# Kernel optimization log

Hardware: AMD Instinct MI355X
Metric: run time of the kernel (lower is better)

The kernel has to match this reference:

```python
import jax, jax.numpy as jnp
import numpy as np

D = 128           # volume / particle box size (pixels)
B = 8             # particles per batch
K = 125           # SO(3) grid poses (5x5x5 around each center Euler)
TOPK = 2          # keep_top_k_values
MAX_SHIFT_FRAC = 0.25  # main_config.projmatching.max_shift_fraction


def setup_inputs() -> dict:
    key = jax.random.key(0)
    k1, k2, k3, k4 = jax.random.split(key, 4)
    vol = jax.random.normal(k1, (D, D, D), dtype=jnp.float32)
    parts = jax.random.normal(k2, (B, D, D), dtype=jnp.float32)
    ctf = jax.random.uniform(k3, (B, D, D // 2 + 1), dtype=jnp.float32)
    euler_degs = jax.random.normal(k4, (K, 3), dtype=jnp.float32) * 8.0
    return {"vol": vol, "parts": parts, "ctf": ctf, "euler_degs": euler_degs}


def _rot_z(t):
    c, s = jnp.cos(t), jnp.sin(t)
    z, o = jnp.zeros_like(t), jnp.ones_like(t)
    return jnp.stack([jnp.stack([c, -s, z], -1),
                      jnp.stack([s, c, z], -1),
                      jnp.stack([z, z, o], -1)], -2)


def _rot_y(t):
    c, s = jnp.cos(t), jnp.sin(t)
    z, o = jnp.zeros_like(t), jnp.ones_like(t)
    return jnp.stack([jnp.stack([c, z, s], -1),
                      jnp.stack([z, o, z], -1),
                      jnp.stack([-s, z, c], -1)], -2)


def euler_zyz_to_matrix(degs):
    # RELION Euler convention ZYZ: R = Rz(a) @ Ry(b) @ Rz(c)
    rad = jnp.deg2rad(degs)
    return _rot_z(rad[..., 0]) @ _rot_y(rad[..., 1]) @ _rot_z(rad[..., 2])


def trilinear_sample(vol, zi, yi, xi):
    # vol: (Dz, Dy, W) complex64; coords: (K, h, w) float32 array indices
    Dz, Dy, W = vol.shape
    z0, y0, x0 = jnp.floor(zi), jnp.floor(yi), jnp.floor(xi)
    tz, ty, tx = zi - z0, yi - y0, xi - x0
    out = jnp.zeros(zi.shape, dtype=vol.dtype)
    for dz in (0, 1):
        wz = tz if dz else 1.0 - tz
        zc = z0 + dz
        vz = (zc >= 0) & (zc < Dz)
        zdx = jnp.clip(zc, 0, Dz - 1).astype(jnp.int32)
        for dy in (0, 1):
            wy = ty if dy else 1.0 - ty
            yc = y0 + dy
            vy = (yc >= 0) & (yc < Dy)
            ydx = jnp.clip(yc, 0, Dy - 1).astype(jnp.int32)
            for dx in (0, 1):
                wx = tx if dx else 1.0 - tx
                xc = x0 + dx
                vx = (xc >= 0) & (xc < W)
                xdx = jnp.clip(xc, 0, W - 1).astype(jnp.int32)
                w = jnp.where(vz & vy & vx, wz * wy * wx, 0.0)
                out = out + w * vol[zdx, ydx, xdx]
    return out


def project_fourier(vol_rfft, rotmats):
    # extract_central_slices_rfft: pose-dependent gather+trilinear interp of a
    # central slice from the fftshifted 3D rfft volume. Output: (K, D, D//2+1).
    d = D
    w = d // 2 + 1
    y = jnp.arange(d, dtype=jnp.float32) - d // 2   # fftshifted full-dim freqs (pixel units)
    x = jnp.arange(w, dtype=jnp.float32)            # rfft (non-negative) freqs
    yy, xx = jnp.meshgrid(y, x, indexing='ij')      # (d, w)
    coords = jnp.stack([xx, yy, jnp.zeros_like(yy)], -1)       # xyz, (d, w, 3), z = 0 plane
    rot = jnp.einsum('kij,hwj->khwi', rotmats, coords)          # (K, d, w, 3) rotated xyz
    conj_mask = rot[..., 0] < 0                                  # Hermitian symmetry: flip to x>=0 half
    rot = jnp.where(conj_mask[..., None], -rot, rot)
    xi = rot[..., 0]
    yi = rot[..., 1] + d // 2
    zi = rot[..., 2] + d // 2
    samples = trilinear_sample(vol_rfft, zi, yi, xi)
    samples = jnp.where(conj_mask, jnp.conj(samples), samples)
    r2 = xx ** 2 + yy ** 2                                       # zero beyond Nyquist radius
    samples = jnp.where(r2[None] > (d // 2) ** 2, 0.0, samples)
    return samples


def reference(vol, parts, ctf, euler_degs):
    # compute_dft: rfft volume, fftshift non-rfft dims
    vol_rfft = jnp.fft.fftshift(jnp.fft.rfftn(vol), axes=(0, 1))
    parts_rfft = jnp.fft.fftshift(jnp.fft.rfft2(parts), axes=(-2,))  # (B, D, W)
    rotmats = euler_zyz_to_matrix(euler_degs)                        # (K, 3, 3)
    projs = project_fourier(vol_rfft, rotmats)                       # (K, D, W)
    projs = ctf[:, None] * projs[None]                               # _apply_ctfF: (B, K, D, W)
    # correlate_dft_2d: cross-correlation via iFFT of parts * conj(projs)
    prod = parts_rfft[:, None] * jnp.conj(projs)
    prod = jnp.fft.ifftshift(prod, axes=(-2,))
    corr = jnp.fft.irfft2(prod, s=(D, D))                            # (B, K, D, D)
    corr = jnp.fft.fftshift(corr, axes=(-2, -1))                     # zero shift at center
    # _extract_ccor_max: restrict to |shift| <= max_shift_fraction*D, take top-k peaks
    center = D // 2
    max_shift = int(MAX_SHIFT_FRAC * D)
    idx = jnp.arange(D) - center
    win = (jnp.abs(idx)[:, None] <= max_shift) & (jnp.abs(idx)[None, :] <= max_shift)
    masked = jnp.where(win, corr, -jnp.inf)
    flat = masked.reshape(B, K, D * D)
    vals, top_idx = jax.lax.top_k(flat, TOPK)                        # (B, K, TOPK)
    shifts = jnp.stack([top_idx // D - center, top_idx % D - center], -1)  # (B, K, TOPK, 2) yx
    return vals, shifts
```

## Files before the change

### kernel.cpp

```cpp
#include <hip/hip_runtime.h>
#include <math.h>

#define D 128
#define W 65
#define NK 125
#define NB 8
#define SLAB (D*W)
#define TWO_PI 6.28318530717958647692f
#define R2C 0.70710678118654752440f
#define C8C 0.92387953251128675613f
#define S8C 0.38268343236508977173f
#define ARS 146
#define GRS 131


__device__ __forceinline__ bool better(float va, int ia, float vb, int ib) {
    return (va > vb) || (va == vb && ia < ib);
}
__device__ __forceinline__ float2 cmul(float2 a, float2 b) {
    return make_float2(a.x*b.x - a.y*b.y, a.x*b.y + a.y*b.x);
}
__device__ __forceinline__ void cmac(float2& acc, float2 a, float2 b) {
    acc.x = fmaf(a.x, b.x, fmaf(-a.y, b.y, acc.x));
    acc.y = fmaf(a.x, b.y, fmaf( a.y, b.x, acc.y));
}
__device__ __forceinline__ float2 cadd(float2 a, float2 b){ return make_float2(a.x+b.x, a.y+b.y); }
__device__ __forceinline__ float2 csub(float2 a, float2 b){ return make_float2(a.x-b.x, a.y-b.y); }

__device__ __forceinline__ void fft8_fwd(const float2* x, float2* a) {
    float2 e0 = x[0], o0 = x[1], e1 = x[2], o1 = x[3];
    float2 e2 = x[4], o2 = x[5], e3 = x[6], o3 = x[7];
    float2 t0 = cadd(e0, e2), t1 = csub(e0, e2);
    float2 t2 = cadd(e1, e3), t3 = csub(e1, e3);
    float2 E0 = cadd(t0, t2), E2 = csub(t0, t2);
    float2 E1 = make_float2(t1.x + t3.y, t1.y - t3.x);
    float2 E3 = make_float2(t1.x - t3.y, t1.y + t3.x);
    float2 u0 = cadd(o0, o2), u1 = csub(o0, o2);
    float2 u2 = cadd(o1, o3), u3 = csub(o1, o3);
    float2 O0 = cadd(u0, u2), O2 = csub(u0, u2);
    float2 O1 = make_float2(u1.x + u3.y, u1.y - u3.x);
    float2 O3 = make_float2(u1.x - u3.y, u1.y + u3.x);
    float2 w1 = make_float2(R2C*(O1.x + O1.y), R2C*(O1.y - O1.x));
    float2 w2 = make_float2(O2.y, -O2.x);
    float2 w3 = make_float2(R2C*(O3.y - O3.x), -R2C*(O3.x + O3.y));
    a[0] = cadd(E0, O0); a[4] = csub(E0, O0);
    a[1] = cadd(E1, w1); a[5] = csub(E1, w1);
    a[2] = cadd(E2, w2); a[6] = csub(E2, w2);
    a[3] = cadd(E3, w3); a[7] = csub(E3, w3);
}

__device__ __forceinline__ void ifft8_reg(const float2* x, float2* a) {
    float2 e0 = x[0], o0 = x[1], e1 = x[2], o1 = x[3];
    float2 e2 = x[4], o2 = x[5], e3 = x[6], o3 = x[7];
    float2 t0 = cadd(e0, e2), t1 = csub(e0, e2);
    float2 t2 = cadd(e1, e3), t3 = csub(e1, e3);
    float2 E0 = cadd(t0, t2), E2 = csub(t0, t2);
    float2 E1 = make_float2(t1.x - t3.y, t1.y + t3.x);
    float2 E3 = make_float2(t1.x + t3.y, t1.y - t3.x);
    float2 u0 = cadd(o0, o2), u1 = csub(o0, o2);
    float2 u2 = cadd(o1, o3), u3 = csub(o1, o3);
    float2 O0 = cadd(u0, u2), O2 = csub(u0, u2);
    float2 O1 = make_float2(u1.x - u3.y, u1.y + u3.x);
    float2 O3 = make_float2(u1.x + u3.y, u1.y - u3.x);
    float2 w1o = make_float2(R2C*(O1.x - O1.y), R2C*(O1.x + O1.y));
    float2 w2o = make_float2(-O2.y, O2.x);
    float2 w3o = make_float2(R2C*(-O3.x - O3.y), R2C*(O3.x - O3.y));
    a[0] = cadd(E0, O0); a[4] = csub(E0, O0);
    a[1] = cadd(E1, w1o); a[5] = csub(E1, w1o);
    a[2] = cadd(E2, w2o); a[6] = csub(E2, w2o);
    a[3] = cadd(E3, w3o); a[7] = csub(E3, w3o);
}


template<int MODE>
__device__ __forceinline__ void fft128v2(const float* __restrict__ inf,
                                         const float2* __restrict__ inc,
                                         float2* __restrict__ out,
                                         const float* __restrict__ ct,
                                         int l0, int nlines,
                                         float2* __restrict__ Fl,
                                         float2* __restrict__ twf) {
    int tid = threadIdx.x;
    int line, t;
    if (MODE == 0) { t = tid & 7; line = tid >> 3; }
    else           { line = tid & 31; t = tid >> 5; }
    int l = l0 + line;
    bool live = (l < nlines);

    if (tid < 128) {
        float s, c;
        sincosf(-TWO_PI * (float)tid / 128.0f, &s, &c);
        twf[tid] = make_float2(c, s);
    }

    int base = 0, stride = 1;
    if (MODE == 1 || MODE == 3 || MODE == 4) { base = (l / W) * SLAB + (l % W); stride = W; }
    else if (MODE == 2) { base = l; stride = SLAB; }

    float2 xe[8], xo[8];
    if (live) {
        if (MODE == 0) {
            const float* r = inf + (size_t)l * D;
            #pragma unroll
            for (int j = 0; j < 8; ++j) {
                xe[j] = make_float2(r[t + 16*j], 0.f);
                xo[j] = make_float2(r[t + 8 + 16*j], 0.f);
            }
        } else {
            #pragma unroll
            for (int j = 0; j < 8; ++j) {
                xe[j] = inc[base + (t + 16*j) * stride];
                xo[j] = inc[base + (t + 8 + 16*j) * stride];
            }
        }
    } else {
        #pragma unroll
        for (int j = 0; j < 8; ++j) { xe[j] = make_float2(0,0); xo[j] = make_float2(0,0); }
    }
    float2 E[8], O[8];
    fft8_fwd(xe, E);
    fft8_fwd(xo, O);
    {
        const float2 w16[8] = {
            { 1.f, 0.f }, { C8C, -S8C }, { R2C, -R2C }, { S8C, -C8C },
            { 0.f, -1.f }, { -S8C, -C8C }, { -R2C, -R2C }, { -C8C, -S8C }
        };
        float2* Fp = Fl + line * 137 + t * 17;
        #pragma unroll
        for (int kk = 0; kk < 8; ++kk) {
            float2 wo = cmul(w16[kk], O[kk]);
            Fp[kk]     = cadd(E[kk], wo);
            Fp[kk + 8] = csub(E[kk], wo);
        }
    }
    __syncthreads();
    if (live) {
        const float2* Fr = Fl + line * 137;
        #pragma unroll
        for (int s = 0; s < 16; ++s) {
            int slot = t + 8 * s;
            if (MODE == 0 && slot > 64) break;
            int k = (MODE == 0) ? slot : (slot ^ 64);
            int kk = k & 15;
            float2 acc = make_float2(0.f, 0.f);
            #pragma unroll
            for (int tt = 0; tt < 8; ++tt) {
                cmac(acc, Fr[tt * 17 + kk], twf[(tt * k) & 127]);
            }
            if (MODE == 0)      out[(size_t)l * W + slot] = acc;
            else if (MODE == 3) out[(size_t)l * D + slot] = acc;
            else if (MODE == 4) {
                float cf = ct[(size_t)l * D + slot];
                out[(size_t)l * D + slot] = make_float2(acc.x * cf, acc.y * cf);
            }
            else                out[base + slot * stride] = acc;
        }
    }
}


__global__ __launch_bounds__(256) void k1_kernel(const float* __restrict__ vol,
                                                 const float* __restrict__ parts,
                                                 const float* __restrict__ ctf,
                                                 const float* __restrict__ euler,
                                                 float2* __restrict__ bufA,
                                                 float2* __restrict__ pT1,
                                                 float* __restrict__ CT,
                                                 float* __restrict__ rot) {
    __shared__ float2 Fl[32 * 137];
    __shared__ float2 twf[128];
    int bid = blockIdx.x;
    int tid = threadIdx.x;
    if (bid < 512) {
        fft128v2<0>(vol, nullptr, bufA, nullptr, bid * 32, D*D, Fl, twf);
    } else if (bid < 544) {
        fft128v2<0>(parts, nullptr, pT1, nullptr, (bid - 512) * 32, NB*D, Fl, twf);
    } else if (bid == 544) {
        int k = tid;
        if (k < NK) {
            const float d2r = 0.017453292519943295f;
            float a = euler[k*3+0]*d2r, b = euler[k*3+1]*d2r, c = euler[k*3+2]*d2r;
            float sa, ca, sb, cb, sc, cc;
            sincosf(a, &sa, &ca); sincosf(b, &sb, &cb); sincosf(c, &sc, &cc);
            rot[k*9+0] =  ca*cb*cc - sa*sc;
            rot[k*9+1] = -ca*cb*sc - sa*cc;
            rot[k*9+2] =  ca*sb;
            rot[k*9+3] =  sa*cb*cc + ca*sc;
            rot[k*9+4] = -sa*cb*sc + ca*cc;
            rot[k*9+5] =  sa*sb;
            rot[k*9+6] = -sb*cc;
            rot[k*9+7] =  sb*sc;
            rot[k*9+8] =  cb;
        }
    } else {
        int i = (bid - 545) * 256 + tid;
        if (i < NB * W * D) {
            int m = i & (D-1);
            int t2 = i >> 7;
            int x = t2 % W;
            int b = t2 / W;
            CT[i] = ctf[b * SLAB + m * W + x];
        }
    }
}

__global__ __launch_bounds__(256) void k2_kernel(const float2* __restrict__ bufA,
                                                 float2* __restrict__ bufB,
                                                 const float2* __restrict__ pT1,
                                                 float2* __restrict__ ST,
                                                 const float* __restrict__ CT) {
    __shared__ float2 Fl[32 * 137];
    __shared__ float2 twf[128];
    int bid = blockIdx.x;
    if (bid < 260) fft128v2<1>(nullptr, bufA, bufB, nullptr, bid * 32, D*W, Fl, twf);
    else           fft128v2<4>(nullptr, pT1, ST, CT, (bid - 260) * 32, NB*W, Fl, twf);
}

__global__ __launch_bounds__(256) void k3_kernel(const float2* __restrict__ bufB,
                                                 float2* __restrict__ bufA) {
    __shared__ float2 Fl[32 * 137];
    __shared__ float2 twf[128];
    fft128v2<2>(nullptr, bufB, bufA, nullptr, blockIdx.x * 32, SLAB, Fl, twf);
}


__global__ void proj_kernel(const float2* __restrict__ vol, const float* __restrict__ rot,
                            float2* __restrict__ projT) {
    int idx = blockIdx.x * blockDim.x + threadIdx.x;
    if (idx >= NK * D * W) return;
    int h = idx & (D-1);
    int t2 = idx >> 7;
    int w = t2 % W;
    int k = t2 / W;
    float x = (float)w;
    float y = (float)(h - 64);
    const float* R = rot + k*9;
    float rx = R[0]*x + R[1]*y;
    float ry = R[3]*x + R[4]*y;
    float rz = R[6]*x + R[7]*y;
    bool neg = rx < 0.0f;
    if (neg) { rx = -rx; ry = -ry; rz = -rz; }
    float xi = rx;
    float yi = ry + 64.0f;
    float zi = rz + 64.0f;
    float z0 = floorf(zi), y0 = floorf(yi), x0 = floorf(xi);
    float tz = zi - z0, ty = yi - y0, tx = xi - x0;
    int z0i = (int)z0, y0i = (int)y0, x0i = (int)x0;
    float ar = 0.f, ai = 0.f;
    for (int dz = 0; dz < 2; ++dz) {
        float wz = dz ? tz : 1.0f - tz;
        int zc = z0i + dz;
        bool vz = (zc >= 0) && (zc < D);
        int zx = min(max(zc, 0), D-1);
        for (int dy = 0; dy < 2; ++dy) {
            float wy = dy ? ty : 1.0f - ty;
            int yc = y0i + dy;
            bool vy = (yc >= 0) && (yc < D);
            int yx = min(max(yc, 0), D-1);
            for (int dx = 0; dx < 2; ++dx) {
                float wx = dx ? tx : 1.0f - tx;
                int xc = x0i + dx;
                bool vx = (xc >= 0) && (xc < W);
                int xx = min(max(xc, 0), W-1);
                float wt = (vz && vy && vx) ? wz*wy*wx : 0.0f;
                float2 v = vol[zx * SLAB + yx * W + xx];
                ar = fmaf(wt, v.x, ar);
                ai = fmaf(wt, v.y, ai);
            }
        }
    }
    if (neg) ai = -ai;
    int yy = h - 64;
    if (w*w + yy*yy > 4096) { ar = 0.f; ai = 0.f; }
    projT[idx] = make_float2(ar, ai);
}


__global__ __launch_bounds__(256, 2) void corr_kernel(const float2* __restrict__ ST,
                                                      const float2* __restrict__ PJT,
                                                      float* __restrict__ outv) {
    __shared__ float2 tw[128];
    __shared__ float2 AbBC[17*ARS];
    __shared__ float2 G[17*GRS];
    __shared__ float  Ny[65];
    __shared__ float  redv[8];
    __shared__ int    redi[8];

    int g = blockIdx.x;
    int logical = (g & 7) * 125 + (g >> 3);
    int k = logical >> 3;
    int b = logical & 7;
    int tid = threadIdx.x;
    const float inv_d = 1.0f / 128.0f;

    if (tid < 128) {
        float s, c;
        sincosf(TWO_PI * (float)tid / 128.0f, &s, &c);
        tw[tid] = make_float2(c, s);
    }

    const float2* Sb = ST + b * (W * D);
    const float2* Jk = PJT + k * (W * D);

    int lane = tid & 63;
    int wv = tid >> 6;
    int sv = lane & 7;
    int vp = (96 + lane) & 127;
    float acc[16];
    #pragma unroll
    for (int j = 0; j < 16; ++j) acc[j] = 0.0f;
    float accR = 0.0f;
    int ur = 0, vr = 0;
    if (tid < 129) { if (tid < 65) { ur = 64; vr = tid; } else { ur = tid - 65; vr = 64; } }

    __syncthreads();

    float2 wvp = tw[vp];
    float2 tq = make_float2(1.0f, 0.0f);

    int l1 = tid >> 4, m01 = tid & 15;
    float2 Sv[8], Jv[8];

    for (int cg = 0; cg < 4; ++cg) {
        if (cg == 0) {
            for (int i = tid; i < 17 * 16; i += 256) {
                int l = i >> 4, m0 = i & 15;
                int x = (l < 16) ? ((l >> 2) + 16 * (l & 3)) : 64;
                const float2* Sx = Sb + x * 128 + m0;
                const float2* Jx = Jk + x * 128 + m0;
                float2 p[8];
                #pragma unroll
                for (int j = 0; j < 8; ++j) {
                    float2 s = Sx[16*j];
                    float2 pj = Jx[16*j];
                    p[j] = make_float2(s.x*pj.x + s.y*pj.y, s.y*pj.x - s.x*pj.y);
                }
                float2 A[8];
                ifft8_reg(p, A);
                float2* dst = AbBC + l * ARS + m0;
                dst[0] = A[0];
                #pragma unroll
                for (int r = 1; r < 8; ++r) dst[r*18] = cmul(A[r], tw[(r * m0) & 127]);
            }
        } else {
            float2 p[8];
            #pragma unroll
            for (int j = 0; j < 8; ++j) {
                p[j] = make_float2(Sv[j].x*Jv[j].x + Sv[j].y*Jv[j].y,
                                   Sv[j].y*Jv[j].x - Sv[j].x*Jv[j].y);
            }
            float2 A[8];
            ifft8_reg(p, A);
            float2* dst = AbBC + l1 * ARS + m01;
            dst[0] = A[0];
            #pragma unroll
            for (int r = 1; r < 8; ++r) dst[r*18] = cmul(A[r], tw[(r * m01) & 127]);
        }
        __syncthreads();
        {
            int lim2 = (cg == 0) ? 136 : 128;
            for (int i = tid; i < lim2; i += 256) {
                int l, r;
                if (i < 128) { l = i & 15; r = i >> 4; }
                else         { l = 16; r = i - 128; }
                const float4* Ar = (const float4*)(AbBC + l * ARS + r * 18);
                float2 xe[8], xo[8];
                #pragma unroll
                for (int j = 0; j < 8; ++j) {
                    float4 a = Ar[j];
                    xe[j] = make_float2(a.x, a.y);
                    xo[j] = make_float2(a.z, a.w);
                }
                float2 E[8], O[8];
                ifft8_reg(xe, E);
                ifft8_reg(xo, O);
                const float2 w16p[8] = {
                    { 1.f, 0.f }, { C8C, S8C }, { R2C, R2C }, { S8C, C8C },
                    { 0.f, 1.f }, { -S8C, C8C }, { -R2C, R2C }, { -C8C, S8C }
                };
                float2* Gl = G + l * GRS + r;
                #pragma unroll
                for (int t = 0; t < 8; ++t) {
                    float2 wo = cmul(w16p[t], O[t]);
                    Gl[8*t]      = cadd(E[t], wo);
                    Gl[8*t + 64] = csub(E[t], wo);
                }
            }
        }
        if (cg < 3) {
            int xn = 4*(cg+1) + (l1 >> 2) + 16 * (l1 & 3);
            const float2* Sx = Sb + xn * 128 + m01;
            const float2* Jx = Jk + xn * 128 + m01;
            #pragma unroll
            for (int j = 0; j < 8; ++j) {
                Sv[j] = Sx[16*j];
                Jv[j] = Jx[16*j];
            }
        }
        __syncthreads();
        {
            float2* BC = AbBC;
            int lim = (cg == 0) ? 325 : 260;
            for (int i = tid; i < lim; i += 256) {
                if (i < 260) {
                    int q = i / 65;
                    int u2 = i - q * 65;
                    int up = (96 + u2) & 127;
                    float sg = (u2 & 1) ? -inv_d : inv_d;
                    const float2* Gq = G + up;
                    float2 h0 = Gq[(4*q+0)*GRS];
                    float2 h1 = Gq[(4*q+1)*GRS];
                    float2 h2 = Gq[(4*q+2)*GRS];
                    float2 h3 = Gq[(4*q+3)*GRS];
                    h0.x *= sg; h0.y *= sg; h1.x *= sg; h1.y *= sg;
                    h2.x *= sg; h2.y *= sg; h3.x *= sg; h3.y *= sg;
                    if (cg == 0 && q == 0) { h0.x *= 0.5f; h0.y *= 0.5f; }
                    const float sc = 2.0f * inv_d;
                    float2 p1 = make_float2(R2C*(h1.x - h1.y), R2C*(h1.x + h1.y));
                    float2 q1 = make_float2(R2C*(-h1.x - h1.y), R2C*(h1.x - h1.y));
                    float2 i1 = make_float2(-h1.y, h1.x);
                    float2 i2 = make_float2(-h2.y, h2.x);
                    float2 n2 = make_float2( h2.y, -h2.x);
                    float2 p3 = make_float2(R2C*(h3.x - h3.y), R2C*(h3.x + h3.y));
                    float2 q3 = make_float2(R2C*(-h3.x - h3.y), R2C*(h3.x - h3.y));
                    float2 i3 = make_float2(-h3.y, h3.x);
                    float2 a02 = cadd(h0, h2), s02 = csub(h0, h2);
                    float2 s0 = cadd(a02, cadd(h1, h3));
                    float2 s4 = csub(a02, cadd(h1, h3));
                    float2 s2 = cadd(s02, csub(i1, i3));
                    float2 s6 = csub(s02, csub(i1, i3));
                    float2 b0i = cadd(h0, i2);
                    float2 b0n = cadd(h0, n2);
                    float2 s1 = cadd(b0i, cadd(p1, q3));
                    float2 s5 = csub(b0i, cadd(p1, q3));
                    float2 s3 = cadd(b0n, cadd(q1, p3));
                    float2 s7 = csub(b0n, cadd(q1, p3));
                    float2* Bp = BC + q * (8*67) + u2;
                    Bp[0*67] = make_float2(s0.x*sc, s0.y*sc);
                    Bp[1*67] = make_float2(s1.x*sc, s1.y*sc);
                    Bp[2*67] = make_float2(s2.x*sc, s2.y*sc);
                    Bp[3*67] = make_float2(s3.x*sc, s3.y*sc);
                    Bp[4*67] = make_float2(s4.x*sc, s4.y*sc);
                    Bp[5*67] = make_float2(s5.x*sc, s5.y*sc);
                    Bp[6*67] = make_float2(s6.x*sc, s6.y*sc);
                    Bp[7*67] = make_float2(s7.x*sc, s7.y*sc);
                } else {
                    int u2 = i - 260;
                    int up = (96 + u2) & 127;
                    Ny[u2] = ((u2 & 1) ? -inv_d : inv_d) * G[16*GRS + up].x;
                }
            }
        }
        __syncthreads();
        {
            const float2* BC = AbBC;
            #pragma unroll
            for (int q = 0; q < 4; ++q) {
                const float2* Bq = BC + (q * 8 + sv) * 67 + wv * 16;
                float tx = tq.x, ty = tq.y;
                #pragma unroll
                for (int j = 0; j < 16; ++j) {
                    float2 bv = Bq[j];
                    acc[j] = fmaf(bv.x, tx, fmaf(-bv.y, ty, acc[j]));
                }
                tq = cmul(tq, wvp);
            }
            if (cg == 0) {
                float sgn = (lane & 1) ? -inv_d : inv_d;
                #pragma unroll
                for (int j = 0; j < 16; ++j) acc[j] = fmaf(sgn, Ny[wv * 16 + j], acc[j]);
            }
            if (tid < 129) {
                int sr = vr & 7, vpr = (96 + vr) & 127;
                float a = accR;
                #pragma unroll
                for (int q = 0; q < 4; ++q) {
                    float2 t = tw[((4*cg + q) * vpr) & 127];
                    float2 bv = AbBC[(q * 8 + sr) * 67 + ur];
                    a = fmaf(bv.x, t.x, fmaf(-bv.y, t.y, a));
                }
                if (cg == 0) a += (vr & 1) ? -inv_d * Ny[ur] : inv_d * Ny[ur];
                accR = a;
            }
        }
        __syncthreads();
    }

    float v1 = -INFINITY, v2 = -INFINITY;
    int i1 = 0x7fffffff, i2 = 0x7fffffff;
    #pragma unroll
    for (int j = 0; j < 16; ++j) {
        float val = acc[j];
        int uu = wv * 16 + j;
        int fl = (32 + uu) * D + (32 + lane);
        if (better(val, fl, v1, i1)) { v2 = v1; i2 = i1; v1 = val; i1 = fl; }
        else if (better(val, fl, v2, i2)) { v2 = val; i2 = fl; }
    }
    if (tid < 129) {
        int fl = (32 + ur) * D + (32 + vr);
        if (better(accR, fl, v1, i1)) { v2 = v1; i2 = i1; v1 = accR; i1 = fl; }
        else if (better(accR, fl, v2, i2)) { v2 = accR; i2 = fl; }
    }
    for (int off = 32; off > 0; off >>= 1) {
        float b1 = __shfl_down(v1, off); int j1 = __shfl_down(i1, off);
        float b2 = __shfl_down(v2, off); int j2 = __shfl_down(i2, off);
        if (better(b1, j1, v1, i1)) {
            float nv2; int ni2;
            if (better(v1, i1, b2, j2)) { nv2 = v1; ni2 = i1; } else { nv2 = b2; ni2 = j2; }
            v1 = b1; i1 = j1; v2 = nv2; i2 = ni2;
        } else {
            if (better(b1, j1, v2, i2)) { v2 = b1; i2 = j1; }
        }
    }
    int wave = tid >> 6;
    if ((tid & 63) == 0) {
        redv[wave*2]   = v1; redi[wave*2]   = i1;
        redv[wave*2+1] = v2; redi[wave*2+1] = i2;
    }
    __syncthreads();
    if (tid == 0) {
        float r1 = -INFINITY, r2 = -INFINITY;
        int q1 = 0x7fffffff, q2 = 0x7fffffff;
        for (int i = 0; i < 8; ++i) {
            float val = redv[i]; int fl = redi[i];
            if (better(val, fl, r1, q1)) { r2 = r1; q2 = q1; r1 = val; q1 = fl; }
            else if (better(val, fl, r2, q2)) { r2 = val; q2 = fl; }
        }
        int base = (b * NK + k) * 2;
        outv[base]     = r1;
        outv[base + 1] = r2;
        float* os = outv + NB*NK*2;
        os[(base    )*2 + 0] = (float)(q1 / D - 64);
        os[(base    )*2 + 1] = (float)(q1 % D - 64);
        os[(base + 1)*2 + 0] = (float)(q2 / D - 64);
        os[(base + 1)*2 + 1] = (float)(q2 % D - 64);
    }
}


extern "C" void kernel_launch(void* const* d_in, const int* in_sizes, int n_in,
                              void* d_out, int out_size, void* d_ws, size_t ws_size,
                              hipStream_t stream) {
    const float* vol   = (const float*)d_in[0];
    const float* parts = (const float*)d_in[1];
    const float* ctf   = (const float*)d_in[2];
    const float* euler = (const float*)d_in[3];
    float* out = (float*)d_out;

    const int VOLC = D * SLAB;
    float2* bufA   = (float2*)d_ws;
    float2* bufB   = bufA + VOLC;
    float2* pT1    = bufB + VOLC;
    float2* ST     = pT1 + NB * SLAB;
    float2* PJT    = ST + NB * W * D;
    float*  CT     = (float*)(PJT + NK * W * D);
    float*  rot    = CT + NB * W * D;

    k1_kernel<<<805, 256, 0, stream>>>(vol, parts, ctf, euler, bufA, pT1, CT, rot);
    k2_kernel<<<277, 256, 0, stream>>>(bufA, bufB, pT1, ST, CT);
    k3_kernel<<<260, 256, 0, stream>>>(bufB, bufA);
    proj_kernel<<<(NK*D*W + 255) / 256, 256, 0, stream>>>(bufA, rot, PJT);
    corr_kernel<<<NB * NK, 256, 0, stream>>>(ST, PJT, out);
}
```

Before: 83.23 us.

## Remap proj blocks across XCDs and compact corr shared-memory layouts

proj_kernel now remaps block IDs so each of the 8 XCDs handles a contiguous span of work-groups, which should keep volume gathers in that XCD's L2. In corr_kernel the G buffer is compacted to store only the 65 needed frequency rows (GS stride), which removes the modular index remap. The B buffer stride goes to 68 so the inner loop can read float4 pairs, and the per-thread twiddles are hoisted into registers. The global prefetch of the next S/J chunk also moves earlier, before the barrier, to overlap it with the column FFT. Together these shift shared-memory bank patterns and add register pressure. The dead MODE 3 path is removed.

New measurement: 82.05 us. About the same (-1.4%).

```diff
diff --git a/kernel.cpp b/kernel.cpp
--- a/kernel.cpp
+++ b/kernel.cpp
@@ -11,7 +11,8 @@
 #define C8C 0.92387953251128675613f
 #define S8C 0.38268343236508977173f
 #define ARS 146
-#define GRS 131
+#define GS  67
+#define BRS 68
 
 
 __device__ __forceinline__ bool better(float va, int ia, float vb, int ib) {
@@ -94,7 +95,7 @@
     }
 
     int base = 0, stride = 1;
-    if (MODE == 1 || MODE == 3 || MODE == 4) { base = (l / W) * SLAB + (l % W); stride = W; }
+    if (MODE == 1 || MODE == 4) { base = (l / W) * SLAB + (l % W); stride = W; }
     else if (MODE == 2) { base = l; stride = SLAB; }
 
     float2 xe[8], xo[8];
@@ -148,7 +149,6 @@
                 cmac(acc, Fr[tt * 17 + kk], twf[(tt * k) & 127]);
             }
             if (MODE == 0)      out[(size_t)l * W + slot] = acc;
-            else if (MODE == 3) out[(size_t)l * D + slot] = acc;
             else if (MODE == 4) {
                 float cf = ct[(size_t)l * D + slot];
                 out[(size_t)l * D + slot] = make_float2(acc.x * cf, acc.y * cf);
@@ -224,9 +224,13 @@
 }
 
 
-__global__ void proj_kernel(const float2* __restrict__ vol, const float* __restrict__ rot,
-                            float2* __restrict__ projT) {
-    int idx = blockIdx.x * blockDim.x + threadIdx.x;
+__global__ __launch_bounds__(256) void proj_kernel(const float2* __restrict__ vol,
+                                                   const float* __restrict__ rot,
+                                                   float2* __restrict__ projT) {
+    int bid = blockIdx.x;
+    int xcd = bid & 7, ii = bid >> 3;
+    int wg = (xcd < 7) ? (xcd * 508 + ii) : (3556 + ii);
+    int idx = wg * 256 + threadIdx.x;
     if (idx >= NK * D * W) return;
     int h = idx & (D-1);
     int t2 = idx >> 7;
@@ -280,8 +284,8 @@
                                                       const float2* __restrict__ PJT,
                                                       float* __restrict__ outv) {
     __shared__ float2 tw[128];
-    __shared__ float2 AbBC[17*ARS];
-    __shared__ float2 G[17*GRS];
+    __shared__ __align__(16) float2 AbBC[17*ARS];
+    __shared__ float2 Gs[17*GS];
     __shared__ float  Ny[65];
     __shared__ float  redv[8];
     __shared__ int    redi[8];
@@ -320,6 +324,10 @@
 
     int l1 = tid >> 4, m01 = tid & 15;
     float2 Sv[8], Jv[8];
+    float2 twr[8];
+    twr[0] = make_float2(1.f, 0.f);
+    #pragma unroll
+    for (int r = 1; r < 8; ++r) twr[r] = tw[(r * m01) & 127];
 
     for (int cg = 0; cg < 4; ++cg) {
         if (cg == 0) {
@@ -354,7 +362,17 @@
             float2* dst = AbBC + l1 * ARS + m01;
             dst[0] = A[0];
             #pragma unroll
-            for (int r = 1; r < 8; ++r) dst[r*18] = cmul(A[r], tw[(r * m01) & 127]);
+            for (int r = 1; r < 8; ++r) dst[r*18] = cmul(A[r], twr[r]);
+        }
+        if (cg < 3) {
+            int xn = 4*(cg+1) + (l1 >> 2) + 16 * (l1 & 3);
+            const float2* Sx = Sb + xn * 128 + m01;
+            const float2* Jx = Jk + xn * 128 + m01;
+            #pragma unroll
+            for (int j = 0; j < 8; ++j) {
+                Sv[j] = Sx[16*j];
+                Jv[j] = Jx[16*j];
+            }
         }
         __syncthreads();
         {
@@ -378,23 +396,17 @@
                     { 1.f, 0.f }, { C8C, S8C }, { R2C, R2C }, { S8C, C8C },
                     { 0.f, 1.f }, { -S8C, C8C }, { -R2C, R2C }, { -C8C, S8C }
                 };
-                float2* Gl = G + l * GRS + r;
+                float2* Gl = Gs + l * GS;
                 #pragma unroll
                 for (int t = 0; t < 8; ++t) {
                     float2 wo = cmul(w16p[t], O[t]);
-                    Gl[8*t]      = cadd(E[t], wo);
-                    Gl[8*t + 64] = csub(E[t], wo);
+                    float2 lowv  = cadd(E[t], wo);
+                    float2 highv = csub(E[t], wo);
+                    int klow = r + 8*t;
+                    if (t <= 3) Gl[klow + 32] = lowv;
+                    if (t == 4 && r == 0) Gl[64] = lowv;
+                    if (t >= 4) Gl[klow - 32] = highv;
                 }
-            }
-        }
-        if (cg < 3) {
-            int xn = 4*(cg+1) + (l1 >> 2) + 16 * (l1 & 3);
-            const float2* Sx = Sb + xn * 128 + m01;
-            const float2* Jx = Jk + xn * 128 + m01;
-            #pragma unroll
-            for (int j = 0; j < 8; ++j) {
-                Sv[j] = Sx[16*j];
-                Jv[j] = Jx[16*j];
             }
         }
         __syncthreads();
@@ -405,13 +417,12 @@
                 if (i < 260) {
                     int q = i / 65;
                     int u2 = i - q * 65;
-                    int up = (96 + u2) & 127;
                     float sg = (u2 & 1) ? -inv_d : inv_d;
-                    const float2* Gq = G + up;
-                    float2 h0 = Gq[(4*q+0)*GRS];
-                    float2 h1 = Gq[(4*q+1)*GRS];
-                    float2 h2 = Gq[(4*q+2)*GRS];
-                    float2 h3 = Gq[(4*q+3)*GRS];
+                    const float2* Gq = Gs + (4*q) * GS + u2;
+                    float2 h0 = Gq[0*GS];
+                    float2 h1 = Gq[1*GS];
+                    float2 h2 = Gq[2*GS];
+                    float2 h3 = Gq[3*GS];
                     h0.x *= sg; h0.y *= sg; h1.x *= sg; h1.y *= sg;
                     h2.x *= sg; h2.y *= sg; h3.x *= sg; h3.y *= sg;
                     if (cg == 0 && q == 0) { h0.x *= 0.5f; h0.y *= 0.5f; }
@@ -435,33 +446,32 @@
                     float2 s5 = csub(b0i, cadd(p1, q3));
                     float2 s3 = cadd(b0n, cadd(q1, p3));
                     float2 s7 = csub(b0n, cadd(q1, p3));
-                    float2* Bp = BC + q * (8*67) + u2;
-                    Bp[0*67] = make_float2(s0.x*sc, s0.y*sc);
-                    Bp[1*67] = make_float2(s1.x*sc, s1.y*sc);
-                    Bp[2*67] = make_float2(s2.x*sc, s2.y*sc);
-                    Bp[3*67] = make_float2(s3.x*sc, s3.y*sc);
-                    Bp[4*67] = make_float2(s4.x*sc, s4.y*sc);
-                    Bp[5*67] = make_float2(s5.x*sc, s5.y*sc);
-                    Bp[6*67] = make_float2(s6.x*sc, s6.y*sc);
-                    Bp[7*67] = make_float2(s7.x*sc, s7.y*sc);
+                    float2* Bp = BC + q * (8*BRS) + u2;
+                    Bp[0*BRS] = make_float2(s0.x*sc, s0.y*sc);
+                    Bp[1*BRS] = make_float2(s1.x*sc, s1.y*sc);
+                    Bp[2*BRS] = make_float2(s2.x*sc, s2.y*sc);
+                    Bp[3*BRS] = make_float2(s3.x*sc, s3.y*sc);
+                    Bp[4*BRS] = make_float2(s4.x*sc, s4.y*sc);
+                    Bp[5*BRS] = make_float2(s5.x*sc, s5.y*sc);
+                    Bp[6*BRS] = make_float2(s6.x*sc, s6.y*sc);
+                    Bp[7*BRS] = make_float2(s7.x*sc, s7.y*sc);
                 } else {
                     int u2 = i - 260;
-                    int up = (96 + u2) & 127;
-                    Ny[u2] = ((u2 & 1) ? -inv_d : inv_d) * G[16*GRS + up].x;
+                    Ny[u2] = ((u2 & 1) ? -inv_d : inv_d) * Gs[16*GS + u2].x;
                 }
             }
         }
         __syncthreads();
         {
-            const float2* BC = AbBC;
             #pragma unroll
             for (int q = 0; q < 4; ++q) {
-                const float2* Bq = BC + (q * 8 + sv) * 67 + wv * 16;
+                const float4* Bq = (const float4*)(AbBC + q * (8*BRS) + sv * BRS + wv * 16);
                 float tx = tq.x, ty = tq.y;
                 #pragma unroll
-                for (int j = 0; j < 16; ++j) {
-                    float2 bv = Bq[j];
-                    acc[j] = fmaf(bv.x, tx, fmaf(-bv.y, ty, acc[j]));
+                for (int jp = 0; jp < 8; ++jp) {
+                    float4 bb = Bq[jp];
+                    acc[2*jp]   = fmaf(bb.x, tx, fmaf(-bb.y, ty, acc[2*jp]));
+                    acc[2*jp+1] = fmaf(bb.z, tx, fmaf(-bb.w, ty, acc[2*jp+1]));
                 }
                 tq = cmul(tq, wvp);
             }
@@ -471,12 +481,13 @@
                 for (int j = 0; j < 16; ++j) acc[j] = fmaf(sgn, Ny[wv * 16 + j], acc[j]);
             }
             if (tid < 129) {
-                int sr = vr & 7, vpr = (96 + vr) & 127;
+                int sr = vr & 7;
+                int vpr = (96 + vr) & 127;
                 float a = accR;
                 #pragma unroll
                 for (int q = 0; q < 4; ++q) {
                     float2 t = tw[((4*cg + q) * vpr) & 127];
-                    float2 bv = AbBC[(q * 8 + sr) * 67 + ur];
+                    float2 bv = AbBC[q * (8*BRS) + sr * BRS + ur];
                     a = fmaf(bv.x, t.x, fmaf(-bv.y, t.y, a));
                 }
                 if (cg == 0) a += (vr & 1) ? -inv_d * Ny[ur] : inv_d * Ny[ur];
@@ -559,6 +570,6 @@
     k1_kernel<<<805, 256, 0, stream>>>(vol, parts, ctf, euler, bufA, pT1, CT, rot);
     k2_kernel<<<277, 256, 0, stream>>>(bufA, bufB, pT1, ST, CT);
     k3_kernel<<<260, 256, 0, stream>>>(bufB, bufA);
-    proj_kernel<<<(NK*D*W + 255) / 256, 256, 0, stream>>>(bufA, rot, PJT);
+    proj_kernel<<<4063, 256, 0, stream>>>(bufA, rot, PJT);
     corr_kernel<<<NB * NK, 256, 0, stream>>>(ST, PJT, out);
 }
```
